# Kernel tuning notes

Measured on AMD Instinct MI355X. Metric: run time of the kernel, lower is better.

## Reference

```python
import jax, jax.numpy as jnp
import numpy as np

EPS = 1e-4
TAU = 0.1
GAMMA = 64.0
RADIUS = 1.0
N_HEADS = 4
N_SPLIT = 4


def _l2norm(x, axis=-1):
    return x / jnp.maximum(jnp.linalg.norm(x, axis=axis, keepdims=True), 1e-12)


def _pd2(a, b):
    # pairwise squared distances: (B,N,M)
    return (jnp.sum(a * a, -1)[:, :, None] + jnp.sum(b * b, -1)[:, None, :]
            - 2.0 * jnp.einsum('bnd,bmd->bnm', a, b))


def _sim_matrix(xyz, nf, radius, gamma):
    # radius-masked Gaussian feature affinity, zero diagonal
    N = xyz.shape[1]
    d2x = _pd2(xyz, xyz)
    d2f = _pd2(nf, nf)
    A = jnp.exp(-gamma * d2f / nf.shape[-1]) * (d2x < radius * radius).astype(nf.dtype)
    return A * (1.0 - jnp.eye(N, dtype=A.dtype))


def _norm_lap(A, eps):
    deg = A.sum(-1)
    dinv = jax.lax.rsqrt(deg + eps)
    na = A * dinv[:, :, None] * dinv[:, None, :]
    lap = jnp.eye(A.shape[1], dtype=A.dtype) - na
    return lap, na


def _mincut(X, na, W1, b1, W2, b2, tau):
    # one GCN layer + temperature softmax soft assignment; pooled = weighted mean
    h = jax.nn.relu(jnp.einsum('bnm,bmc->bnc', na, X) @ W1 + b1)
    s = jax.nn.softmax((h @ W2 + b2) / tau, axis=-1)  # (B,N,K)
    denom = s.sum(1)[:, :, None] + EPS                # (B,K,1)
    c_fea = jnp.einsum('bnk,bnc->bkc', s, X) / denom
    return c_fea, s


def _centers(xyz, s):
    denom = s.sum(1)[:, :, None] + EPS
    return jnp.einsum('bnk,bnd->bkd', s, xyz) / denom


def _assignment_loss(p_xyz, c_xyz, s):
    d2 = _pd2(p_xyz, c_xyz)
    return jnp.mean(jnp.sum(s * d2, -1))


def _welsch(p_xyz, c_xyz, sigma):
    d2min = jnp.min(_pd2(p_xyz, c_xyz), -1)
    return jnp.mean(1.0 - jnp.exp(-d2min / (2.0 * sigma * sigma)))


def _knn_affinity(xyz, k):
    N = xyz.shape[1]
    d2 = _pd2(xyz, xyz)
    eye = jnp.eye(N, dtype=d2.dtype)
    neg = -(d2 + 1e6 * eye)
    thresh = jax.lax.top_k(neg, k)[0][..., -1:]
    mask = (neg >= thresh).astype(d2.dtype)
    A = jnp.exp(-d2) * mask * (1.0 - eye)
    return jnp.maximum(A, jnp.swapaxes(A, 1, 2))


def _cut_loss(na, xyz, alpha):
    N = xyz.shape[1]
    lap = jnp.eye(N, dtype=na.dtype) - na
    quad = jnp.einsum('bnd,bnm,bmd->b', xyz, lap, xyz)
    return alpha * jnp.mean(quad / N)


def _cross_attn(gf, cf, Wq, Wk, Wv, Wo, n_heads):
    B, N, C = gf.shape
    M = cf.shape[1]
    dh = C // n_heads
    q = (gf @ Wq).reshape(B, N, n_heads, dh)
    k = (cf @ Wk).reshape(B, M, n_heads, dh)
    v = (cf @ Wv).reshape(B, M, n_heads, dh)
    scores = jnp.einsum('bnhd,bmhd->bhnm', q, k) / np.sqrt(dh).astype(np.float32)
    attn = jax.nn.softmax(scores, -1)
    out = jnp.einsum('bhnm,bmhd->bnhd', attn, v).reshape(B, N, C) @ Wo
    return out, attn.mean(1)


def setup_inputs() -> dict:
    key = jax.random.key(0)
    ks = jax.random.split(key, 20)
    B, N_sp, C, H, K = 2, 1024, 256, 128, 64
    Kg = K // N_SPLIT
    sc = 1.0 / np.sqrt(C)
    sh = 1.0 / np.sqrt(H)
    return {
        'g_fea': jax.random.normal(ks[0], (B, N_sp, C), jnp.float32),
        'g_xyz': jax.random.uniform(ks[1], (B, N_sp, 3), jnp.float32),
        'p_fea_0': jax.random.normal(ks[2], (B, 4096, C), jnp.float32),
        'p_xyz_0': jax.random.uniform(ks[3], (B, 4096, 3), jnp.float32),
        'p_fea_1': jax.random.normal(ks[4], (B, 2048, C), jnp.float32),
        'p_xyz_1': jax.random.uniform(ks[5], (B, 2048, 3), jnp.float32),
        'lW1': jax.random.normal(ks[6], (C, H), jnp.float32) * sc,
        'lb1': jnp.zeros((H,), jnp.float32),
        'lW2': jax.random.normal(ks[7], (H, K), jnp.float32) * sh,
        'lb2': jnp.zeros((K,), jnp.float32),
        'gW1': jax.random.normal(ks[8], (C, H), jnp.float32) * sc,
        'gb1': jnp.zeros((H,), jnp.float32),
        'gW2': jax.random.normal(ks[9], (H, Kg), jnp.float32) * sh,
        'gb2': jnp.zeros((Kg,), jnp.float32),
        'Wq': jax.random.normal(ks[10], (C, C), jnp.float32) * sc,
        'Wk': jax.random.normal(ks[11], (C, C), jnp.float32) * sc,
        'Wv': jax.random.normal(ks[12], (C, C), jnp.float32) * sc,
        'Wo': jax.random.normal(ks[13], (C, C), jnp.float32) * sc,
    }


def reference(g_fea, g_xyz, p_fea_0, p_xyz_0, p_fea_1, p_xyz_1,
              lW1, lb1, lW2, lb2, gW1, gb1, gW2, gb2, Wq, Wk, Wv, Wo):
    l_loss = jnp.zeros((), jnp.float32)
    cx_list, cf_list = [], []
    for p_xyz_i, p_fea_i in ((p_xyz_0, p_fea_0), (p_xyz_1, p_fea_1)):
        nf = _l2norm(p_fea_i)
        A = _sim_matrix(p_xyz_i, nf, RADIUS, GAMMA)
        na = _norm_lap(A, EPS)[1]
        c_fea_i, s_i = _mincut(p_fea_i, na, lW1, lb1, lW2, lb2, TAU)
        c_xyz_i = _centers(p_xyz_i, s_i)
        c2p = jnp.einsum('bnk,bkc->bnc', s_i, jax.lax.stop_gradient(c_fea_i))
        l_loss = l_loss + _assignment_loss(p_xyz_i, c_xyz_i, s_i)
        l_loss = l_loss + jnp.linalg.norm(_l2norm(c2p) - nf) + _welsch(p_xyz_i, c_xyz_i, 1.0)
        cx_list.append(c_xyz_i)
        cf_list.append(c_fea_i)
    c_xyz = jnp.concatenate(cx_list, 1)
    c_fea = jnp.concatenate(cf_list, 1)
    A_c = _knn_affinity(c_xyz, 2 * N_SPLIT)
    na_c = _norm_lap(A_c, EPS)[1]
    c_fea_g, gs = _mincut(c_fea, na_c, gW1, gb1, gW2, gb2, TAU)
    c_xyz_g = _centers(c_xyz, gs)
    cut_loss_c = _assignment_loss(c_xyz, c_xyz_g, gs)
    agg, G_t = _cross_attn(g_fea, c_fea_g, Wq, Wk, Wv, Wo, N_HEADS)
    A_g = _sim_matrix(g_xyz, _l2norm(g_fea), 4.0 * RADIUS, GAMMA)
    ass_loss = _cut_loss(_norm_lap(A_g, EPS)[1], g_xyz, 1e-4)
    g_loss = jnp.mean(jnp.sum(jnp.linalg.norm(_l2norm(agg) - _l2norm(g_fea), axis=-1), 1)) + ass_loss
    return agg, l_loss + cut_loss_c, g_loss
```

## Files before the change

### kernel.cpp

```cpp
#include <hip/hip_runtime.h>

#define EPSF 1e-4f

typedef __attribute__((ext_vector_type(8))) short bf16x8;
typedef __attribute__((ext_vector_type(4))) float f32x4;

__device__ __forceinline__ unsigned short f2bf(float f){
    unsigned int u = __float_as_uint(f);
    return (unsigned short)((u + 0x7FFF + ((u >> 16) & 1)) >> 16);
}
__device__ __forceinline__ float bf2f(unsigned short u){
    return __uint_as_float(((unsigned int)u) << 16);
}
__device__ __forceinline__ float waveSum(float v){
    #pragma unroll
    for (int o = 32; o; o >>= 1) v += __shfl_xor(v, o, 64);
    return v;
}
__device__ __forceinline__ float waveMin(float v){
    #pragma unroll
    for (int o = 32; o; o >>= 1) v = fminf(v, __shfl_xor(v, o, 64));
    return v;
}
__device__ __forceinline__ float waveMax(float v){
    #pragma unroll
    for (int o = 32; o; o >>= 1) v = fmaxf(v, __shfl_xor(v, o, 64));
    return v;
}
__device__ __forceinline__ float blockReduceSum(float v, float* red, int nthr){
    int t = threadIdx.x;
    red[t] = v; __syncthreads();
    for (int s = nthr >> 1; s > 0; s >>= 1){
        if (t < s) red[t] += red[t + s];
        __syncthreads();
    }
    float r = red[0]; __syncthreads();
    return r;
}

__global__ void l2norm_kernel(const float* __restrict__ x, unsigned short* __restrict__ outb, int rows){
    __shared__ float red[256];
    int row = blockIdx.x, t = threadIdx.x;
    float v = x[(long)row*256 + t];
    float s = blockReduceSum(v*v, red, 256);
    float nrm = fmaxf(sqrtf(s), 1e-12f);
    outb[(long)row*256 + t] = f2bf(v / nrm);
}

__global__ void cvt_bf16_kernel(const float* __restrict__ in, unsigned short* __restrict__ out, long n4){
    long i = (long)blockIdx.x*256 + threadIdx.x;
    if (i < n4){
        float4 v = ((const float4*)in)[i];
        unsigned int lo = f2bf(v.x) | ((unsigned int)f2bf(v.y) << 16);
        unsigned int hi = f2bf(v.z) | ((unsigned int)f2bf(v.w) << 16);
        uint2 u; u.x = lo; u.y = hi;
        ((uint2*)out)[i] = u;
    }
}

__global__ void tcvt_kernel(const float* __restrict__ W, unsigned short* __restrict__ WT,
                            int Rw, int Cw){
    __shared__ float tile[64][65];
    int r0 = blockIdx.x*64, c0 = blockIdx.y*64;
    int t = threadIdx.x;
    for (int idx = t; idx < 4096; idx += 256){
        int rr = idx >> 6, cc = idx & 63;
        tile[rr][cc] = (r0+rr < Rw && c0+cc < Cw) ? W[(long)(r0+rr)*Cw + c0+cc] : 0.f;
    }
    __syncthreads();
    for (int idx = t; idx < 4096; idx += 256){
        int cc = idx >> 6, rr = idx & 63;
        if (r0+rr < Rw && c0+cc < Cw)
            WT[(long)(c0+cc)*Rw + r0+rr] = f2bf(tile[rr][cc]);
    }
}

__global__ __launch_bounds__(256) void gram_mfma_kernel(const unsigned short* __restrict__ nf,
                                                        const float* __restrict__ xyz,
                                                        unsigned short* __restrict__ A,
                                                        float* __restrict__ deg,
                                                        int N, float r2, float scale){
    __shared__ short tA[128*40], tB[128*40];
    __shared__ float xa[384], xb[384];
    int tid = threadIdx.x;
    int n0 = blockIdx.y*128, m0 = blockIdx.x*128;
    for (int i = tid; i < 384; i += 256){ xa[i] = xyz[n0*3 + i]; xb[i] = xyz[m0*3 + i]; }
    int w = tid >> 6, l = tid & 63;
    int wy = w >> 1, wx = w & 1;
    int lg = l >> 4, lr = l & 15;
    int srow = tid >> 2, sc = tid & 3;
    f32x4 zero = {0.f, 0.f, 0.f, 0.f};
    f32x4 acc[4][4];
    #pragma unroll
    for (int i = 0; i < 4; ++i)
        #pragma unroll
        for (int j = 0; j < 4; ++j) acc[i][j] = zero;
    for (int kt = 0; kt < 256; kt += 32){
        __syncthreads();
        #pragma unroll
        for (int p = 0; p < 2; ++p){
            int row = srow + p*64;
            uint4 va = *(const uint4*)(nf + (long)(n0+row)*256 + kt + sc*8);
            uint4 vb = *(const uint4*)(nf + (long)(m0+row)*256 + kt + sc*8);
            *(uint4*)(tA + row*40 + sc*8) = va;
            *(uint4*)(tB + row*40 + sc*8) = vb;
        }
        __syncthreads();
        bf16x8 af[4], bfr[4];
        #pragma unroll
        for (int f = 0; f < 4; ++f){
            af[f]  = *(const bf16x8*)(tA + (wy*64 + f*16 + lr)*40 + lg*8);
            bfr[f] = *(const bf16x8*)(tB + (wx*64 + f*16 + lr)*40 + lg*8);
        }
        #pragma unroll
        for (int i = 0; i < 4; ++i)
            #pragma unroll
            for (int j = 0; j < 4; ++j)
                acc[i][j] = __builtin_amdgcn_mfma_f32_16x16x32_bf16(af[i], bfr[j], acc[i][j], 0, 0, 0);
    }
    #pragma unroll
    for (int fi = 0; fi < 4; ++fi){
        #pragma unroll
        for (int r = 0; r < 4; ++r){
            int n_ = wy*64 + fi*16 + lg*4 + r;
            int gn = n0 + n_;
            float rowacc = 0.f;
            #pragma unroll
            for (int fj = 0; fj < 4; ++fj){
                int m_ = wx*64 + fj*16 + lr;
                float dx = xa[n_*3+0]-xb[m_*3+0];
                float dy = xa[n_*3+1]-xb[m_*3+1];
                float dz = xa[n_*3+2]-xb[m_*3+2];
                float d2x = dx*dx + dy*dy + dz*dz;
                int gm = m0 + m_;
                float dot = acc[fi][fj][r];
                float val = (d2x < r2 && gn != gm) ? expf(scale*(2.f*dot - 2.f)) : 0.f;
                A[(long)gn*N + gm] = f2bf(val);
                rowacc += val;
            }
            rowacc += __shfl_xor(rowacc, 1, 64);
            rowacc += __shfl_xor(rowacc, 2, 64);
            rowacc += __shfl_xor(rowacc, 4, 64);
            rowacc += __shfl_xor(rowacc, 8, 64);
            if (lr == 0) atomicAdd(&deg[gn], rowacc);
        }
    }
}

__global__ __launch_bounds__(256) void transpose_scale_kernel(const float* __restrict__ fea,
                                                              const float* __restrict__ deg,
                                                              unsigned short* __restrict__ feaT,
                                                              unsigned short* __restrict__ xsT, int N){
    __shared__ float tile[64][65];
    __shared__ float dl[64];
    int m0 = blockIdx.x*64, c0 = blockIdx.y*64;
    int t = threadIdx.x;
    int lr = t >> 2, lc = (t & 3)*16;
    #pragma unroll
    for (int j = 0; j < 4; ++j){
        float4 v = *(const float4*)(fea + (long)(m0+lr)*256 + c0 + lc + j*4);
        tile[lr][lc+j*4+0] = v.x; tile[lr][lc+j*4+1] = v.y;
        tile[lr][lc+j*4+2] = v.z; tile[lr][lc+j*4+3] = v.w;
    }
    if (t < 64) dl[t] = rsqrtf(deg[m0+t] + EPSF);
    __syncthreads();
    unsigned short vr[16] __attribute__((aligned(16)));
    unsigned short vs[16] __attribute__((aligned(16)));
    #pragma unroll
    for (int j = 0; j < 16; ++j){
        float raw = tile[lc+j][lr];
        vr[j] = f2bf(raw);
        vs[j] = f2bf(raw * dl[lc+j]);
    }
    long off = (long)(c0+lr)*N + m0 + lc;
    *(uint4*)(feaT + off)     = *(uint4*)&vr[0];
    *(uint4*)(feaT + off + 8) = *(uint4*)&vr[8];
    *(uint4*)(xsT + off)      = *(uint4*)&vs[0];
    *(uint4*)(xsT + off + 8)  = *(uint4*)&vs[8];
}

__global__ __launch_bounds__(256) void ax_mfma_kernel(const unsigned short* __restrict__ A,
                                                      const unsigned short* __restrict__ xsT,
                                                      float* __restrict__ PY, int N, int split){
    __shared__ short tA[128*40], tB[64*40];
    int tid = threadIdx.x;
    int c0 = blockIdx.x*64, n0 = blockIdx.y*128;
    int chunk = blockIdx.z;
    int L = N/split, kbase = chunk*L, kend = kbase + L;
    int w = tid >> 6, l = tid & 63;
    int wy = w >> 1, wx = w & 1;
    int lg = l >> 4, lr = l & 15;
    int srow = tid >> 2, sc = tid & 3;
    f32x4 zero = {0.f, 0.f, 0.f, 0.f};
    f32x4 acc[4][2];
    #pragma unroll
    for (int i = 0; i < 4; ++i)
        #pragma unroll
        for (int j = 0; j < 2; ++j) acc[i][j] = zero;
    uint4 pva[2], pvb;
    #pragma unroll
    for (int p = 0; p < 2; ++p)
        pva[p] = *(const uint4*)(A + (long)(n0+srow+p*64)*N + kbase + sc*8);
    pvb = *(const uint4*)(xsT + (long)(c0+srow)*N + kbase + sc*8);
    for (int kt = kbase; kt < kend; kt += 32){
        __syncthreads();
        #pragma unroll
        for (int p = 0; p < 2; ++p)
            *(uint4*)(tA + (srow+p*64)*40 + sc*8) = pva[p];
        *(uint4*)(tB + srow*40 + sc*8) = pvb;
        __syncthreads();
        if (kt + 32 < kend){
            #pragma unroll
            for (int p = 0; p < 2; ++p)
                pva[p] = *(const uint4*)(A + (long)(n0+srow+p*64)*N + kt + 32 + sc*8);
            pvb = *(const uint4*)(xsT + (long)(c0+srow)*N + kt + 32 + sc*8);
        }
        bf16x8 af[4], bfr[2];
        #pragma unroll
        for (int f = 0; f < 4; ++f)
            af[f] = *(const bf16x8*)(tA + (wy*64 + f*16 + lr)*40 + lg*8);
        #pragma unroll
        for (int f = 0; f < 2; ++f)
            bfr[f] = *(const bf16x8*)(tB + (wx*32 + f*16 + lr)*40 + lg*8);
        #pragma unroll
        for (int i = 0; i < 4; ++i)
            #pragma unroll
            for (int j = 0; j < 2; ++j)
                acc[i][j] = __builtin_amdgcn_mfma_f32_16x16x32_bf16(af[i], bfr[j], acc[i][j], 0, 0, 0);
    }
    float* out = PY + (long)chunk*N*256;
    #pragma unroll
    for (int fi = 0; fi < 4; ++fi){
        #pragma unroll
        for (int fj = 0; fj < 2; ++fj){
            #pragma unroll
            for (int r = 0; r < 4; ++r){
                int n_ = n0 + wy*64 + fi*16 + lg*4 + r;
                int c_ = c0 + wx*32 + fj*16 + lr;
                out[(long)n_*256 + c_] = acc[fi][fj][r];
            }
        }
    }
}

__global__ void combine_kernel(const float* __restrict__ PY, const float* __restrict__ deg,
                               unsigned short* __restrict__ Yb, int N, int split){
    long i = (long)blockIdx.x*256 + threadIdx.x;
    long e = i*8;
    float4 s0 = {0,0,0,0}, s1 = {0,0,0,0};
    for (int q = 0; q < split; ++q){
        const float4* p = (const float4*)(PY + (long)q*N*256 + e);
        float4 a = p[0], b = p[1];
        s0.x += a.x; s0.y += a.y; s0.z += a.z; s0.w += a.w;
        s1.x += b.x; s1.y += b.y; s1.z += b.z; s1.w += b.w;
    }
    float d = rsqrtf(deg[e >> 8] + EPSF);
    unsigned short vb[8] __attribute__((aligned(16)));
    vb[0] = f2bf(s0.x*d); vb[1] = f2bf(s0.y*d);
    vb[2] = f2bf(s0.z*d); vb[3] = f2bf(s0.w*d);
    vb[4] = f2bf(s1.x*d); vb[5] = f2bf(s1.y*d);
    vb[6] = f2bf(s1.z*d); vb[7] = f2bf(s1.w*d);
    *(uint4*)(Yb + e) = *(uint4*)vb;
}

__global__ __launch_bounds__(256) void gemm_XW_mfma_kernel(const unsigned short* __restrict__ X,
                                                           const unsigned short* __restrict__ WT,
                                                           const float* __restrict__ bias,
                                                           float* __restrict__ outF,
                                                           unsigned short* __restrict__ outB,
                                                           int R, int Ci, int Co, int relu){
    __shared__ short tA[128*40], tB[128*40];
    int tid = threadIdx.x;
    int c0 = blockIdx.x*128, r0 = blockIdx.y*128;
    int w = tid >> 6, l = tid & 63;
    int wy = w >> 1, wx = w & 1;
    int lg = l >> 4, lr = l & 15;
    int srow = tid >> 2, sc = tid & 3;
    f32x4 zero = {0.f, 0.f, 0.f, 0.f};
    f32x4 acc[4][4];
    #pragma unroll
    for (int i = 0; i < 4; ++i)
        #pragma unroll
        for (int j = 0; j < 4; ++j) acc[i][j] = zero;
    uint4 pva[2], pvb[2];
    #pragma unroll
    for (int p = 0; p < 2; ++p){
        int row = srow + p*64;
        int ar = r0 + row, br = c0 + row;
        pva[p] = (ar < R)  ? *(const uint4*)(X  + (long)ar*Ci + sc*8) : (uint4){0,0,0,0};
        pvb[p] = (br < Co) ? *(const uint4*)(WT + (long)br*Ci + sc*8) : (uint4){0,0,0,0};
    }
    for (int kt = 0; kt < Ci; kt += 32){
        __syncthreads();
        #pragma unroll
        for (int p = 0; p < 2; ++p){
            int row = srow + p*64;
            *(uint4*)(tA + row*40 + sc*8) = pva[p];
            *(uint4*)(tB + row*40 + sc*8) = pvb[p];
        }
        __syncthreads();
        if (kt + 32 < Ci){
            #pragma unroll
            for (int p = 0; p < 2; ++p){
                int row = srow + p*64;
                int ar = r0 + row, br = c0 + row;
                pva[p] = (ar < R)  ? *(const uint4*)(X  + (long)ar*Ci + kt + 32 + sc*8) : (uint4){0,0,0,0};
                pvb[p] = (br < Co) ? *(const uint4*)(WT + (long)br*Ci + kt + 32 + sc*8) : (uint4){0,0,0,0};
            }
        }
        bf16x8 af[4], bfr[4];
        #pragma unroll
        for (int f = 0; f < 4; ++f){
            af[f]  = *(const bf16x8*)(tA + (wy*64 + f*16 + lr)*40 + lg*8);
            bfr[f] = *(const bf16x8*)(tB + (wx*64 + f*16 + lr)*40 + lg*8);
        }
        #pragma unroll
        for (int i = 0; i < 4; ++i)
            #pragma unroll
            for (int j = 0; j < 4; ++j)
                acc[i][j] = __builtin_amdgcn_mfma_f32_16x16x32_bf16(af[i], bfr[j], acc[i][j], 0, 0, 0);
    }
    #pragma unroll
    for (int fi = 0; fi < 4; ++fi){
        #pragma unroll
        for (int fj = 0; fj < 4; ++fj){
            #pragma unroll
            for (int r = 0; r < 4; ++r){
                int rr = r0 + wy*64 + fi*16 + lg*4 + r;
                int cc = c0 + wx*64 + fj*16 + lr;
                if (rr < R && cc < Co){
                    float v = acc[fi][fj][r] + (bias ? bias[cc] : 0.f);
                    if (relu) v = fmaxf(v, 0.f);
                    if (outF) outF[(long)rr*Co + cc] = v;
                    if (outB) outB[(long)rr*Co + cc] = f2bf(v);
                }
            }
        }
    }
}

__global__ __launch_bounds__(256) void gemm_splitk_kernel(const float* __restrict__ X,
                                                          const float* __restrict__ W0,
                                                          const float* __restrict__ W1,
                                                          float* __restrict__ part,
                                                          int R, int Ci, int Co, int Ks){
    __shared__ float sa[32][65], sb[32][65];
    int tid = threadIdx.x, tx = tid & 15, ty = tid >> 4;
    int c0 = blockIdx.x * 64, r0 = blockIdx.y * 64;
    int z = blockIdx.z;
    const float* W = (z / Ks) ? W1 : W0;
    int kchunk = Ci / Ks, kst = (z % Ks) * kchunk;
    float acc[4][4] = {};
    for (int kt = kst; kt < kst + kchunk; kt += 32){
        #pragma unroll
        for (int p = 0; p < 8; ++p){
            int idx = p*256 + tid;
            int k = idx & 31, i = idx >> 5;
            int rr = r0 + i;
            sa[k][i] = (rr < R) ? X[(long)rr*Ci + kt + k] : 0.f;
            int j = idx & 63, kk = idx >> 6;
            int cc = c0 + j;
            sb[kk][j] = (cc < Co) ? W[(long)(kt+kk)*Co + cc] : 0.f;
        }
        __syncthreads();
        #pragma unroll
        for (int k = 0; k < 32; ++k){
            float a0=sa[k][ty*4+0],a1=sa[k][ty*4+1],a2=sa[k][ty*4+2],a3=sa[k][ty*4+3];
            float b0=sb[k][tx*4+0],b1=sb[k][tx*4+1],b2=sb[k][tx*4+2],b3=sb[k][tx*4+3];
            acc[0][0]+=a0*b0; acc[0][1]+=a0*b1; acc[0][2]+=a0*b2; acc[0][3]+=a0*b3;
            acc[1][0]+=a1*b0; acc[1][1]+=a1*b1; acc[1][2]+=a1*b2; acc[1][3]+=a1*b3;
            acc[2][0]+=a2*b0; acc[2][1]+=a2*b1; acc[2][2]+=a2*b2; acc[2][3]+=a2*b3;
            acc[3][0]+=a3*b0; acc[3][1]+=a3*b1; acc[3][2]+=a3*b2; acc[3][3]+=a3*b3;
        }
        __syncthreads();
    }
    float* outp = part + (long)z*R*Co;
    #pragma unroll
    for (int r = 0; r < 4; ++r){
        #pragma unroll
        for (int c = 0; c < 4; ++c){
            int rr = r0 + ty*4 + r, cc = c0 + tx*4 + c;
            if (rr < R && cc < Co) outp[(long)rr*Co + cc] = acc[r][c];
        }
    }
}

__global__ void combine_bias_kernel(const float* __restrict__ part, const float* __restrict__ bias,
                                    float* __restrict__ out, int R, int Co, int Ks, int relu){
    long i = (long)blockIdx.x*256 + threadIdx.x;
    if (i < (long)R*Co){
        long zs = (long)R*Co;
        float s = 0.f;
        for (int q = 0; q < Ks; ++q) s += part[q*zs + i];
        float v = s + (bias ? bias[i % Co] : 0.f);
        if (relu) v = fmaxf(v, 0.f);
        out[i] = v;
    }
}

__global__ __launch_bounds__(256) void softmaxT_kernel(float* __restrict__ s,
                                                       unsigned short* __restrict__ sT,
                                                       int sStride, float invtau){
    __shared__ unsigned short st[64][65];
    int blk = blockIdx.x, t = threadIdx.x, w = t >> 6, l = t & 63;
    #pragma unroll
    for (int i = 0; i < 16; ++i){
        int rloc = w + 4*i;
        long row = (long)blk*64 + rloc;
        float v = s[row*64 + l] * invtau;
        float mx = waveMax(v);
        float e = expf(v - mx);
        float sum = waveSum(e);
        float p = e / sum;
        s[row*64 + l] = p;
        st[l][rloc] = f2bf(p);
    }
    __syncthreads();
    int k = t >> 2, j = (t & 3)*16;
    unsigned short vbuf[16] __attribute__((aligned(16)));
    #pragma unroll
    for (int q = 0; q < 16; ++q) vbuf[q] = st[k][j+q];
    long off = (long)k*sStride + (long)blk*64 + j;
    *(uint4*)(sT + off)     = *(uint4*)&vbuf[0];
    *(uint4*)(sT + off + 8) = *(uint4*)&vbuf[8];
}

__global__ __launch_bounds__(256) void stx_mfma_kernel(const unsigned short* __restrict__ sT,
                                                       const unsigned short* __restrict__ feaT,
                                                       float* __restrict__ part,
                                                       int N, int split, int sStride){
    __shared__ short tA[64*40], tB[256*40];
    int tid = threadIdx.x;
    int z = blockIdx.x, b = z / split, chunk = z % split;
    int L = N / split, kst = chunk * L;
    const unsigned short* sTb = sT + (long)b*N;
    const unsigned short* fT  = feaT + (long)b*256*N;
    int w = tid >> 6, l = tid & 63;
    int lg = l >> 4, lr = l & 15;
    f32x4 zero = {0.f, 0.f, 0.f, 0.f};
    f32x4 acc[4][4];
    #pragma unroll
    for (int i = 0; i < 4; ++i)
        #pragma unroll
        for (int j = 0; j < 4; ++j) acc[i][j] = zero;
    int srow = tid >> 2, koff = (tid & 3)*8;
    for (int kt = kst; kt < kst + L; kt += 32){
        __syncthreads();
        *(uint4*)(tA + srow*40 + koff) = *(const uint4*)(sTb + (long)srow*sStride + kt + koff);
        #pragma unroll
        for (int p = 0; p < 4; ++p){
            int row = srow + p*64;
            *(uint4*)(tB + row*40 + koff) = *(const uint4*)(fT + (long)row*N + kt + koff);
        }
        __syncthreads();
        bf16x8 af[4], bfr[4];
        #pragma unroll
        for (int f = 0; f < 4; ++f){
            af[f]  = *(const bf16x8*)(tA + (f*16 + lr)*40 + lg*8);
            bfr[f] = *(const bf16x8*)(tB + (w*64 + f*16 + lr)*40 + lg*8);
        }
        #pragma unroll
        for (int i = 0; i < 4; ++i)
            #pragma unroll
            for (int j = 0; j < 4; ++j)
                acc[i][j] = __builtin_amdgcn_mfma_f32_16x16x32_bf16(af[i], bfr[j], acc[i][j], 0, 0, 0);
    }
    float* outp = part + (long)z*64*256;
    #pragma unroll
    for (int fi = 0; fi < 4; ++fi){
        #pragma unroll
        for (int fj = 0; fj < 4; ++fj){
            #pragma unroll
            for (int r = 0; r < 4; ++r){
                int kc = fi*16 + lg*4 + r;
                int cc = w*64 + fj*16 + lr;
                outp[(long)kc*256 + cc] = acc[fi][fj][r];
            }
        }
    }
}

__global__ void softmax_kernel(float* __restrict__ x, int Kc, float tau){
    int row = blockIdx.x, lane = threadIdx.x;
    bool act = lane < Kc;
    float v = act ? x[(long)row*Kc + lane] / tau : -1e30f;
    float mx = v;
    #pragma unroll
    for (int o = 32; o; o >>= 1) mx = fmaxf(mx, __shfl_xor(mx, o, 64));
    float e = act ? expf(v - mx) : 0.f;
    float s = e;
    #pragma unroll
    for (int o = 32; o; o >>= 1) s += __shfl_xor(s, o, 64);
    if (act) x[(long)row*Kc + lane] = e / s;
}

__global__ void cluster_xyz_kernel(const float* __restrict__ s, const float* __restrict__ xyz,
                                   float* __restrict__ outx, float* __restrict__ outd,
                                   int N, int Kc, int xBS, int dBS){
    __shared__ float red[256];
    int b = blockIdx.y, k = blockIdx.x, t = threadIdx.x;
    s   += (long)b*N*Kc;
    xyz += (long)b*N*3;
    float a0=0,a1=0,a2=0,ad=0;
    for (int n = t; n < N; n += 256){
        float sv = s[(long)n*Kc + k];
        ad += sv;
        a0 += sv*xyz[n*3+0]; a1 += sv*xyz[n*3+1]; a2 += sv*xyz[n*3+2];
    }
    a0 = blockReduceSum(a0, red, 256);
    a1 = blockReduceSum(a1, red, 256);
    a2 = blockReduceSum(a2, red, 256);
    ad = blockReduceSum(ad, red, 256);
    if (t == 0){
        outx[b*xBS + k*3+0] = a0;
        outx[b*xBS + k*3+1] = a1;
        outx[b*xBS + k*3+2] = a2;
        outd[b*dBS + k] = ad;
    }
}

__global__ __launch_bounds__(256) void gemm_sTX_kernel(const float* __restrict__ s,
                                                       const float* __restrict__ X,
                                                       float* __restrict__ part,
                                                       int N, int Kc, int split,
                                                       long sBS, long xBS){
    __shared__ float sa[32][65], sb[32][65];
    int tid = threadIdx.x, tx = tid & 15, ty = tid >> 4;
    int c0 = blockIdx.x * 64;
    int b = blockIdx.z / split, chunk = blockIdx.z % split;
    int L = N / split, nst = chunk * L;
    s += b*sBS; X += b*xBS;
    float* out = part + (long)blockIdx.z * Kc * 256;
    float acc[4][4] = {};
    for (int nt = nst; nt < nst + L; nt += 32){
        #pragma unroll
        for (int p = 0; p < 8; ++p){
            int idx = p*256 + tid;
            int i = idx & 63, k = idx >> 6;
            sa[k][i] = (i < Kc) ? s[(long)(nt+k)*Kc + i] : 0.f;
            int j = idx & 63, kk = idx >> 6;
            sb[kk][j] = X[(long)(nt+kk)*256 + c0 + j];
        }
        __syncthreads();
        #pragma unroll
        for (int k = 0; k < 32; ++k){
            float a0=sa[k][ty*4+0],a1=sa[k][ty*4+1],a2=sa[k][ty*4+2],a3=sa[k][ty*4+3];
            float b0=sb[k][tx*4+0],b1=sb[k][tx*4+1],b2=sb[k][tx*4+2],b3=sb[k][tx*4+3];
            acc[0][0]+=a0*b0; acc[0][1]+=a0*b1; acc[0][2]+=a0*b2; acc[0][3]+=a0*b3;
            acc[1][0]+=a1*b0; acc[1][1]+=a1*b1; acc[1][2]+=a1*b2; acc[1][3]+=a1*b3;
            acc[2][0]+=a2*b0; acc[2][1]+=a2*b1; acc[2][2]+=a2*b2; acc[2][3]+=a2*b3;
            acc[3][0]+=a3*b0; acc[3][1]+=a3*b1; acc[3][2]+=a3*b2; acc[3][3]+=a3*b3;
        }
        __syncthreads();
    }
    #pragma unroll
    for (int r = 0; r < 4; ++r){
        int kc = ty*4 + r;
        if (kc < Kc){
            #pragma unroll
            for (int c = 0; c < 4; ++c)
                out[(long)kc*256 + c0 + tx*4 + c] = acc[r][c];
        }
    }
}

__global__ void divide_sum_kernel(const float* __restrict__ part, const float* __restrict__ den,
                                  float* __restrict__ cfea, float* __restrict__ cxyz,
                                  int Kc, int split, int fBS, int xBS, int dBS){
    int b = blockIdx.y, k = blockIdx.x, t = threadIdx.x;
    float d = den[b*dBS + k] + EPSF;
    float s = 0.f;
    for (int q = 0; q < split; ++q)
        s += part[((long)(b*split+q)*Kc + k)*256 + t];
    cfea[(long)b*fBS + k*256 + t] = s / d;
    if (t < 3) cxyz[b*xBS + k*3 + t] /= d;
}

__global__ __launch_bounds__(256) void level_loss_kernel(const float* __restrict__ s,
                                                         const float* __restrict__ pxyz,
                                                         const float* __restrict__ cxyz,
                                                         const float* __restrict__ cfea,
                                                         const unsigned short* __restrict__ nfb,
                                                         float* __restrict__ scal,
                                                         int N, float inv, int ndsSlot){
    __shared__ float cf[64*256];
    __shared__ float cx[192];
    __shared__ float partA[4], partN[4];
    int b = blockIdx.y, t = threadIdx.x, w = t >> 6, l = t & 63;
    s    += (long)b*N*64;
    pxyz += (long)b*N*3;
    nfb  += (long)b*N*256;
    cxyz += (long)b*384;
    cfea += (long)b*32768;
    for (int i = t; i < 4096; i += 256)
        ((float4*)cf)[i] = ((const float4*)cfea)[i];
    if (t < 192) cx[t] = cxyz[t];
    __syncthreads();
    int n = blockIdx.x*4 + w;
    float sl = s[(long)n*64 + l];
    float px = pxyz[n*3+0], py = pxyz[n*3+1], pz = pxyz[n*3+2];
    float dx = px - cx[l*3+0], dy = py - cx[l*3+1], dz = pz - cx[l*3+2];
    float d2 = dx*dx + dy*dy + dz*dz;
    float assSum = waveSum(sl*d2);
    float dmin = waveMin(d2);
    float c0=0,c1=0,c2=0,c3=0;
    #pragma unroll 8
    for (int k = 0; k < 64; ++k){
        float sk = __shfl(sl, k, 64);
        const float* row = cf + k*256;
        c0 += sk*row[l]; c1 += sk*row[l+64]; c2 += sk*row[l+128]; c3 += sk*row[l+192];
    }
    float nrm2 = waveSum(c0*c0 + c1*c1 + c2*c2 + c3*c3);
    float inrm = 1.f / fmaxf(sqrtf(nrm2), 1e-12f);
    const unsigned short* nfr = nfb + (long)n*256;
    float e0 = c0*inrm - bf2f(nfr[l]);
    float e1 = c1*inrm - bf2f(nfr[l+64]);
    float e2 = c2*inrm - bf2f(nfr[l+128]);
    float e3 = c3*inrm - bf2f(nfr[l+192]);
    float nds = waveSum(e0*e0 + e1*e1 + e2*e2 + e3*e3);
    if (l == 0){
        partA[w] = inv*(assSum + 1.f - expf(-0.5f*dmin));
        partN[w] = nds;
    }
    __syncthreads();
    if (t == 0){
        int slot = blockIdx.x & 63;
        atomicAdd(&scal[slot], partA[0]+partA[1]+partA[2]+partA[3]);
        atomicAdd(&scal[ndsSlot*64 + slot], partN[0]+partN[1]+partN[2]+partN[3]);
    }
}

__global__ __launch_bounds__(128) void knn_nac_kernel(const float* __restrict__ cxyz,
                                                      float* __restrict__ nac){
    __shared__ float d2s[128][129];
    __shared__ float x[128][3];
    __shared__ float di[128];
    int b = blockIdx.x, n = threadIdx.x;
    x[n][0] = cxyz[b*384 + n*3+0];
    x[n][1] = cxyz[b*384 + n*3+1];
    x[n][2] = cxyz[b*384 + n*3+2];
    __syncthreads();
    float xn0 = x[n][0], xn1 = x[n][1], xn2 = x[n][2];
    for (int m = 0; m < 128; ++m){
        float dx = xn0-x[m][0], dy = xn1-x[m][1], dz = xn2-x[m][2];
        d2s[n][m] = dx*dx+dy*dy+dz*dz + (m==n ? 1e6f : 0.f);
    }
    float last = -1.f;
    for (int p = 0; p < 8; ++p){
        float cur = 1e30f;
        for (int m = 0; m < 128; ++m){
            float v = d2s[n][m];
            if (v > last && v < cur) cur = v;
        }
        last = cur;
    }
    for (int m = 0; m < 128; ++m){
        float d2 = d2s[n][m];
        d2s[n][m] = (m != n && d2 <= last) ? expf(-d2) : 0.f;
    }
    __syncthreads();
    for (int m = 0; m < 128; ++m){
        float v = fmaxf(d2s[n][m], d2s[m][n]);
        d2s[n][m] = v;
    }
    __syncthreads();
    float deg = 0.f;
    for (int m = 0; m < 128; ++m) deg += d2s[n][m];
    di[n] = rsqrtf(deg + EPSF);
    __syncthreads();
    float* Ab = nac + (long)b*16384;
    for (int c = 0; c < 128; ++c)
        Ab[c*128 + n] = d2s[c][n] * di[c] * di[n];
}

__global__ void bmm_small_kernel(const float* __restrict__ nac, const float* __restrict__ cfea,
                                 float* __restrict__ Y2){
    __shared__ float row[128];
    int b = blockIdx.y, n = blockIdx.x, t = threadIdx.x;
    if (t < 128) row[t] = nac[(long)b*16384 + n*128 + t];
    __syncthreads();
    float acc = 0.f;
    #pragma unroll 4
    for (int k = 0; k < 128; ++k) acc += row[k]*cfea[(long)b*32768 + k*256 + t];
    Y2[(long)b*32768 + n*256 + t] = acc;
}

__global__ void cutc_kernel(const float* __restrict__ gs, const float* __restrict__ cxyz,
                            const float* __restrict__ cxyzg, float* __restrict__ scal, float inv){
    __shared__ float cg[48];
    __shared__ float red[128];
    int b = blockIdx.x, t = threadIdx.x;
    if (t < 48) cg[t] = cxyzg[b*48 + t];
    __syncthreads();
    float x0 = cxyz[b*384 + t*3+0], x1 = cxyz[b*384 + t*3+1], x2 = cxyz[b*384 + t*3+2];
    float acc = 0.f;
    #pragma unroll
    for (int k = 0; k < 16; ++k){
        float dx = x0-cg[k*3+0], dy = x1-cg[k*3+1], dz = x2-cg[k*3+2];
        acc += gs[b*2048 + t*16 + k]*(dx*dx+dy*dy+dz*dz);
    }
    acc = blockReduceSum(acc, red, 128);
    if (t == 0) atomicAdd(&scal[b], acc*inv);
}

__global__ __launch_bounds__(256) void attn_kernel(const float* __restrict__ q,
                                                   const float* __restrict__ kk,
                                                   const float* __restrict__ vv,
                                                   unsigned short* __restrict__ aob){
    __shared__ float Ks[16][256], Vs[16][256];
    int b = blockIdx.y, n = blockIdx.x, t = threadIdx.x;
    #pragma unroll
    for (int p = 0; p < 16; ++p){
        int j = p*256 + t;
        Ks[j>>8][j&255] = kk[b*4096 + j];
        Vs[j>>8][j&255] = vv[b*4096 + j];
    }
    __syncthreads();
    float qv = q[((long)b*1024 + n)*256 + t];
    float sc[16];
    #pragma unroll
    for (int m = 0; m < 16; ++m){
        float v = qv * Ks[m][t];
        #pragma unroll
        for (int o = 32; o; o >>= 1) v += __shfl_xor(v, o, 64);
        sc[m] = v * 0.125f;
    }
    float mx = -1e30f;
    #pragma unroll
    for (int m = 0; m < 16; ++m) mx = fmaxf(mx, sc[m]);
    float sum = 0.f;
    #pragma unroll
    for (int m = 0; m < 16; ++m){ sc[m] = expf(sc[m]-mx); sum += sc[m]; }
    float o = 0.f;
    #pragma unroll
    for (int m = 0; m < 16; ++m) o += sc[m]*Vs[m][t];
    aob[((long)b*1024 + n)*256 + t] = f2bf(o / sum);
}

__global__ void quad_kernel(const unsigned short* __restrict__ A, const float* __restrict__ deg,
                            const float* __restrict__ xyz, float* __restrict__ scal){
    __shared__ float part[4];
    int t = threadIdx.x, w = t >> 6, l = t & 63;
    int n = blockIdx.x*4 + w;
    float a0=0,a1=0,a2=0;
    #pragma unroll 4
    for (int i = 0; i < 16; ++i){
        int m = l + i*64;
        float wv = bf2f(A[(long)n*1024 + m])*rsqrtf(deg[m] + EPSF);
        a0 += wv*xyz[m*3+0]; a1 += wv*xyz[m*3+1]; a2 += wv*xyz[m*3+2];
    }
    a0 = waveSum(a0); a1 = waveSum(a1); a2 = waveSum(a2);
    if (l == 0){
        float x0 = xyz[n*3+0], x1 = xyz[n*3+1], x2 = xyz[n*3+2];
        float dn = rsqrtf(deg[n] + EPSF);
        part[w] = (x0*x0+x1*x1+x2*x2) - dn*(x0*a0+x1*a1+x2*a2);
    }
    __syncthreads();
    if (t == 0) atomicAdd(&scal[4*64 + (blockIdx.x & 63)], part[0]+part[1]+part[2]+part[3]);
}

__global__ void gloss_kernel(const float* __restrict__ agg, const float* __restrict__ gfea,
                             float* __restrict__ scal){
    __shared__ float part[4];
    int t = threadIdx.x, w = t >> 6, l = t & 63;
    long r = (long)blockIdx.x*4 + w;
    const float* a = agg + r*256;
    const float* g = gfea + r*256;
    float a0=a[l],a1=a[l+64],a2=a[l+128],a3=a[l+192];
    float g0=g[l],g1=g[l+64],g2=g[l+128],g3=g[l+192];
    float na2 = waveSum(a0*a0+a1*a1+a2*a2+a3*a3);
    float ng2 = waveSum(g0*g0+g1*g1+g2*g2+g3*g3);
    float ia = 1.f/fmaxf(sqrtf(na2), 1e-12f), ig = 1.f/fmaxf(sqrtf(ng2), 1e-12f);
    float e0=a0*ia-g0*ig, e1=a1*ia-g1*ig, e2=a2*ia-g2*ig, e3=a3*ia-g3*ig;
    float d2 = waveSum(e0*e0+e1*e1+e2*e2+e3*e3);
    if (l == 0) part[w] = sqrtf(d2);
    __syncthreads();
    if (t == 0) atomicAdd(&scal[3*64 + (blockIdx.x & 63)], part[0]+part[1]+part[2]+part[3]);
}

__global__ void finalize_kernel(const float* __restrict__ scal, float* __restrict__ out){
    int t = threadIdx.x;
    float s[5];
    #pragma unroll
    for (int q = 0; q < 5; ++q){
        float v = scal[q*64 + t];
        #pragma unroll
        for (int o = 32; o; o >>= 1) v += __shfl_xor(v, o, 64);
        s[q] = v;
    }
    if (t == 0){
        out[524288] = s[0] + sqrtf(s[1]) + sqrtf(s[2]);
        out[524289] = s[3]*0.5f + 1e-4f*s[4]/2048.0f;
    }
}

extern "C" void kernel_launch(void* const* d_in, const int* in_sizes, int n_in,
                              void* d_out, int out_size, void* d_ws, size_t ws_size,
                              hipStream_t stream){
    const float* g_fea   = (const float*)d_in[0];
    const float* g_xyz   = (const float*)d_in[1];
    const float* p_fea_0 = (const float*)d_in[2];
    const float* p_xyz_0 = (const float*)d_in[3];
    const float* p_fea_1 = (const float*)d_in[4];
    const float* p_xyz_1 = (const float*)d_in[5];
    const float* lW1 = (const float*)d_in[6];
    const float* lb1 = (const float*)d_in[7];
    const float* lW2 = (const float*)d_in[8];
    const float* lb2 = (const float*)d_in[9];
    const float* gW1 = (const float*)d_in[10];
    const float* gb1 = (const float*)d_in[11];
    const float* gW2 = (const float*)d_in[12];
    const float* gb2 = (const float*)d_in[13];
    const float* Wq = (const float*)d_in[14];
    const float* Wk = (const float*)d_in[15];
    const float* Wv = (const float*)d_in[16];
    const float* Wo = (const float*)d_in[17];
    float* out = (float*)d_out;
    float* ws_f = (float*)d_ws;

    constexpr long O_SCALS = 0;
    constexpr long O_DEG   = 512;
    constexpr long O_CFEA  = 16384;
    constexpr long O_CXYZ  = 81920;
    constexpr long O_DEN   = 82688;
    constexpr long O_CFG   = 82944;
    constexpr long O_CXG   = 91136;
    constexpr long O_DENG  = 91232;
    constexpr long O_NFB   = 91296;
    constexpr long O_XST   = O_NFB  + 1572864;
    constexpr long O_FEAT  = O_XST  + 1048576;
    constexpr long O_YB    = O_FEAT + 1572864;
    constexpr long O_HB    = O_YB   + 1572864;
    constexpr long O_S     = O_HB   + 786432;
    constexpr long O_ST    = O_S    + 786432;
    constexpr long O_PY    = O_ST   + 393216;
    constexpr long O_A     = O_PY   + 8388608;
    constexpr long O_Q     = O_A    + 8388608;
    constexpr long O_GFB   = O_Q    + 524288;
    constexpr long O_AOB   = O_GFB  + 262144;
    constexpr long O_KK    = O_AOB  + 262144;
    constexpr long O_VV    = O_KK   + 8192;
    constexpr long O_NAC   = O_VV   + 8192;
    constexpr long O_Y2    = O_NAC  + 32768;
    constexpr long O_H2    = O_Y2   + 65536;
    constexpr long O_LG2   = O_H2   + 32768;
    constexpr long O_W1T   = O_LG2  + 4096;
    constexpr long O_W2T   = O_W1T  + 16384;
    constexpr long O_WQT   = O_W2T  + 4096;
    constexpr long O_WOT   = O_WQT  + 32768;

    hipMemsetAsync(ws_f + O_SCALS, 0, (512 + 14336)*sizeof(float), stream);

    unsigned short* nfb  = (unsigned short*)(ws_f + O_NFB);
    unsigned short* xsT  = (unsigned short*)(ws_f + O_XST);
    unsigned short* feaT = (unsigned short*)(ws_f + O_FEAT);
    unsigned short* Ybb  = (unsigned short*)(ws_f + O_YB);
    unsigned short* Hb   = (unsigned short*)(ws_f + O_HB);
    unsigned short* sTb  = (unsigned short*)(ws_f + O_ST);
    unsigned short* A    = (unsigned short*)(ws_f + O_A);
    unsigned short* gfb  = (unsigned short*)(ws_f + O_GFB);
    unsigned short* aob  = (unsigned short*)(ws_f + O_AOB);
    unsigned short* lW1T = (unsigned short*)(ws_f + O_W1T);
    unsigned short* lW2T = (unsigned short*)(ws_f + O_W2T);
    unsigned short* WqT  = (unsigned short*)(ws_f + O_WQT);
    unsigned short* WoT  = (unsigned short*)(ws_f + O_WOT);
    float* sb   = ws_f + O_S;
    float* degA = ws_f + O_DEG;
    float* PY   = ws_f + O_PY;
    float* Qf   = ws_f + O_Q;

    tcvt_kernel<<<dim3(4, 2), 256, 0, stream>>>(lW1, lW1T, 256, 128);
    tcvt_kernel<<<dim3(2, 1), 256, 0, stream>>>(lW2, lW2T, 128, 64);
    tcvt_kernel<<<dim3(4, 4), 256, 0, stream>>>(Wq, WqT, 256, 256);
    tcvt_kernel<<<dim3(4, 4), 256, 0, stream>>>(Wo, WoT, 256, 256);
    cvt_bf16_kernel<<<512, 256, 0, stream>>>(g_fea, gfb, 131072);

    struct Lvl { const float* fea; const float* xyz; int N; int k0; int ndsSlot; long degBase;
                 long rowOff; long featOff; };
    Lvl lv[2] = {{p_fea_0, p_xyz_0, 4096, 0, 1, 0, 0, 0},
                 {p_fea_1, p_xyz_1, 2048, 64, 2, 8192, 8192, 2097152}};

    for (int L = 0; L < 2; ++L){
        int N = lv[L].N;
        const float* fea = lv[L].fea;
        const float* xyz = lv[L].xyz;
        unsigned short* nfbL  = nfb + lv[L].rowOff*256;
        unsigned short* feaTL = feaT + lv[L].featOff;
        l2norm_kernel<<<2*N, 256, 0, stream>>>(fea, nfbL, 2*N);
        for (int b = 0; b < 2; ++b){
            float* degb = degA + lv[L].degBase + (long)b*N;
            gram_mfma_kernel<<<dim3(N/128, N/128), 256, 0, stream>>>(nfbL + (long)b*N*256,
                                                                     xyz + (long)b*N*3, A, degb,
                                                                     N, 1.0f, 0.25f);
            transpose_scale_kernel<<<dim3(N/64, 4), 256, 0, stream>>>(fea + (long)b*N*256, degb,
                                                                      feaTL + (long)b*256*N,
                                                                      xsT + (long)b*256*N, N);
            ax_mfma_kernel<<<dim3(4, N/128, 8), 256, 0, stream>>>(A, xsT + (long)b*256*N, PY, N, 8);
            combine_kernel<<<N/8, 256, 0, stream>>>(PY, degb,
                                                    Ybb + (lv[L].rowOff + (long)b*N)*256, N, 8);
        }
    }

    gemm_XW_mfma_kernel<<<dim3(1, 96), 256, 0, stream>>>(Ybb, lW1T, lb1, nullptr, Hb,
                                                         12288, 256, 128, 1);
    gemm_XW_mfma_kernel<<<dim3(1, 96), 256, 0, stream>>>(Hb, lW2T, lb2, sb, nullptr,
                                                         12288, 128, 64, 0);
    softmaxT_kernel<<<192, 256, 0, stream>>>(sb, sTb, 12288, 10.0f);

    for (int L = 0; L < 2; ++L){
        int N = lv[L].N;
        const float* xyz = lv[L].xyz;
        float* sL = sb + lv[L].rowOff*64;
        cluster_xyz_kernel<<<dim3(64, 2), 256, 0, stream>>>(sL, xyz, ws_f + O_CXYZ + lv[L].k0*3,
                                                            ws_f + O_DEN + lv[L].k0, N, 64, 384, 128);
        stx_mfma_kernel<<<32, 256, 0, stream>>>(sTb + lv[L].rowOff, feaT + lv[L].featOff,
                                                PY, N, 16, 12288);
        divide_sum_kernel<<<dim3(64, 2), 256, 0, stream>>>(PY, ws_f + O_DEN + lv[L].k0,
                                                           ws_f + O_CFEA + lv[L].k0*256,
                                                           ws_f + O_CXYZ + lv[L].k0*3,
                                                           64, 16, 128*256, 384, 128);
        level_loss_kernel<<<dim3(N/4, 2), 256, 0, stream>>>(sL, xyz, ws_f + O_CXYZ + lv[L].k0*3,
                                                            ws_f + O_CFEA + lv[L].k0*256,
                                                            nfb + lv[L].rowOff*256,
                                                            ws_f + O_SCALS, N, 1.0f/(2.0f*N), lv[L].ndsSlot);
    }

    knn_nac_kernel<<<2, 128, 0, stream>>>(ws_f + O_CXYZ, ws_f + O_NAC);
    bmm_small_kernel<<<dim3(128, 2), 256, 0, stream>>>(ws_f + O_NAC, ws_f + O_CFEA, ws_f + O_Y2);
    gemm_splitk_kernel<<<dim3(2, 4, 4), 256, 0, stream>>>(ws_f + O_Y2, gW1, nullptr, PY,
                                                          256, 256, 128, 4);
    combine_bias_kernel<<<128, 256, 0, stream>>>(PY, gb1, ws_f + O_H2, 256, 128, 4, 1);
    gemm_splitk_kernel<<<dim3(1, 4, 4), 256, 0, stream>>>(ws_f + O_H2, gW2, nullptr, PY,
                                                          256, 128, 16, 4);
    combine_bias_kernel<<<16, 256, 0, stream>>>(PY, gb2, ws_f + O_LG2, 256, 16, 4, 0);
    softmax_kernel<<<256, 64, 0, stream>>>(ws_f + O_LG2, 16, 0.1f);
    cluster_xyz_kernel<<<dim3(16, 2), 256, 0, stream>>>(ws_f + O_LG2, ws_f + O_CXYZ,
                                                        ws_f + O_CXG, ws_f + O_DENG, 128, 16, 48, 16);
    gemm_sTX_kernel<<<dim3(4, 1, 8), 256, 0, stream>>>(ws_f + O_LG2, ws_f + O_CFEA, PY,
                                                       128, 16, 4, 128L*16, 128L*256);
    divide_sum_kernel<<<dim3(16, 2), 256, 0, stream>>>(PY, ws_f + O_DENG, ws_f + O_CFG,
                                                       ws_f + O_CXG, 16, 4, 16*256, 48, 16);
    cutc_kernel<<<2, 128, 0, stream>>>(ws_f + O_LG2, ws_f + O_CXYZ, ws_f + O_CXG,
                                       ws_f + O_SCALS, 1.0f/256.0f);

    gemm_XW_mfma_kernel<<<dim3(2, 16), 256, 0, stream>>>(gfb, WqT, nullptr, Qf, nullptr,
                                                         2048, 256, 256, 0);
    gemm_splitk_kernel<<<dim3(4, 1, 16), 256, 0, stream>>>(ws_f + O_CFG, Wk, Wv, PY,
                                                           32, 256, 256, 8);
    combine_bias_kernel<<<32, 256, 0, stream>>>(PY, nullptr, ws_f + O_KK, 32, 256, 8, 0);
    combine_bias_kernel<<<32, 256, 0, stream>>>(PY + 8L*32*256, nullptr, ws_f + O_VV, 32, 256, 8, 0);
    attn_kernel<<<dim3(1024, 2), 256, 0, stream>>>(Qf, ws_f + O_KK, ws_f + O_VV, aob);
    gemm_XW_mfma_kernel<<<dim3(2, 16), 256, 0, stream>>>(aob, WoT, nullptr, out, nullptr,
                                                         2048, 256, 256, 0);

    l2norm_kernel<<<2048, 256, 0, stream>>>(g_fea, nfb, 2048);
    for (int b = 0; b < 2; ++b){
        float* degb = degA + 12288 + (long)b*1024;
        gram_mfma_kernel<<<dim3(8, 8), 256, 0, stream>>>(nfb + (long)b*1024*256, g_xyz + (long)b*1024*3,
                                                         A, degb, 1024, 16.0f, 0.25f);
        quad_kernel<<<256, 256, 0, stream>>>(A, degb, g_xyz + (long)b*1024*3, ws_f + O_SCALS);
    }

    gloss_kernel<<<512, 256, 0, stream>>>(out, g_fea, ws_f + O_SCALS);
    finalize_kernel<<<1, 64, 0, stream>>>(ws_f + O_SCALS, out);
}
```

Measured before the change: 756.8 us.

## Widen A·X tile to 128 columns and store split-K partials as bf16

The A·X MFMA kernel now computes a 128x128 output tile per block instead of 128x64. That halves how often the large affinity matrix A is read across column blocks and doubles the MFMA work per LDS fill. Split-K partial sums are staged through shared memory and written as bf16 with coalesced 16-byte stores, and combine_kernel reads them as bf16, which halves partial-sum traffic. The cost is more accumulator registers, which may lower occupancy, and some precision lost by rounding each partial to bf16 before the sum.

Result: faster. 739.1 us (-2.3%).

```diff
diff --git a/kernel.cpp b/kernel.cpp
--- a/kernel.cpp
+++ b/kernel.cpp
@@ -181,10 +181,12 @@
 
 __global__ __launch_bounds__(256) void ax_mfma_kernel(const unsigned short* __restrict__ A,
                                                       const unsigned short* __restrict__ xsT,
-                                                      float* __restrict__ PY, int N, int split){
-    __shared__ short tA[128*40], tB[64*40];
+                                                      unsigned short* __restrict__ PYb, int N, int split){
+    __shared__ short smem[16384];
+    short* tA = smem;
+    short* tB = smem + 5120;
     int tid = threadIdx.x;
-    int c0 = blockIdx.x*64, n0 = blockIdx.y*128;
+    int c0 = blockIdx.x*128, n0 = blockIdx.y*128;
     int chunk = blockIdx.z;
     int L = N/split, kbase = chunk*L, kend = kbase + L;
     int w = tid >> 6, l = tid & 63;
@@ -192,74 +194,89 @@
     int lg = l >> 4, lr = l & 15;
     int srow = tid >> 2, sc = tid & 3;
     f32x4 zero = {0.f, 0.f, 0.f, 0.f};
-    f32x4 acc[4][2];
+    f32x4 acc[4][4];
     #pragma unroll
     for (int i = 0; i < 4; ++i)
         #pragma unroll
-        for (int j = 0; j < 2; ++j) acc[i][j] = zero;
-    uint4 pva[2], pvb;
-    #pragma unroll
-    for (int p = 0; p < 2; ++p)
-        pva[p] = *(const uint4*)(A + (long)(n0+srow+p*64)*N + kbase + sc*8);
-    pvb = *(const uint4*)(xsT + (long)(c0+srow)*N + kbase + sc*8);
+        for (int j = 0; j < 4; ++j) acc[i][j] = zero;
+    uint4 pva[2], pvb[2];
+    #pragma unroll
+    for (int p = 0; p < 2; ++p){
+        int row = srow + p*64;
+        pva[p] = *(const uint4*)(A   + (long)(n0+row)*N + kbase + sc*8);
+        pvb[p] = *(const uint4*)(xsT + (long)(c0+row)*N + kbase + sc*8);
+    }
     for (int kt = kbase; kt < kend; kt += 32){
         __syncthreads();
         #pragma unroll
-        for (int p = 0; p < 2; ++p)
-            *(uint4*)(tA + (srow+p*64)*40 + sc*8) = pva[p];
-        *(uint4*)(tB + srow*40 + sc*8) = pvb;
+        for (int p = 0; p < 2; ++p){
+            int row = srow + p*64;
+            *(uint4*)(tA + row*40 + sc*8) = pva[p];
+            *(uint4*)(tB + row*40 + sc*8) = pvb[p];
+        }
         __syncthreads();
         if (kt + 32 < kend){
             #pragma unroll
-            for (int p = 0; p < 2; ++p)
-                pva[p] = *(const uint4*)(A + (long)(n0+srow+p*64)*N + kt + 32 + sc*8);
-            pvb = *(const uint4*)(xsT + (long)(c0+srow)*N + kt + 32 + sc*8);
-        }
-        bf16x8 af[4], bfr[2];
-        #pragma unroll
-        for (int f = 0; f < 4; ++f)
-            af[f] = *(const bf16x8*)(tA + (wy*64 + f*16 + lr)*40 + lg*8);
-        #pragma unroll
-        for (int f = 0; f < 2; ++f)
-            bfr[f] = *(const bf16x8*)(tB + (wx*32 + f*16 + lr)*40 + lg*8);
+            for (int p = 0; p < 2; ++p){
+                int row = srow + p*64;
+                pva[p] = *(const uint4*)(A   + (long)(n0+row)*N + kt + 32 + sc*8);
+                pvb[p] = *(const uint4*)(xsT + (long)(c0+row)*N + kt + 32 + sc*8);
+            }
+        }
+        bf16x8 af[4], bfr[4];
+        #pragma unroll
+        for (int f = 0; f < 4; ++f){
+            af[f]  = *(const bf16x8*)(tA + (wy*64 + f*16 + lr)*40 + lg*8);
+            bfr[f] = *(const bf16x8*)(tB + (wx*64 + f*16 + lr)*40 + lg*8);
+        }
         #pragma unroll
         for (int i = 0; i < 4; ++i)
             #pragma unroll
-            for (int j = 0; j < 2; ++j)
+            for (int j = 0; j < 4; ++j)
                 acc[i][j] = __builtin_amdgcn_mfma_f32_16x16x32_bf16(af[i], bfr[j], acc[i][j], 0, 0, 0);
     }
-    float* out = PY + (long)chunk*N*256;
+    __syncthreads();
+    unsigned short* ot = (unsigned short*)smem;
     #pragma unroll
     for (int fi = 0; fi < 4; ++fi){
         #pragma unroll
-        for (int fj = 0; fj < 2; ++fj){
+        for (int fj = 0; fj < 4; ++fj){
             #pragma unroll
             for (int r = 0; r < 4; ++r){
-                int n_ = n0 + wy*64 + fi*16 + lg*4 + r;
-                int c_ = c0 + wx*32 + fj*16 + lr;
-                out[(long)n_*256 + c_] = acc[fi][fj][r];
+                int n_ = wy*64 + fi*16 + lg*4 + r;
+                int c_ = wx*64 + fj*16 + lr;
+                ot[n_*128 + c_] = f2bf(acc[fi][fj][r]);
             }
         }
     }
-}
-
-__global__ void combine_kernel(const float* __restrict__ PY, const float* __restrict__ deg,
+    __syncthreads();
+    unsigned short* outp = PYb + (long)chunk*N*256;
+    #pragma unroll
+    for (int q = 0; q < 8; ++q){
+        int idx = q*256 + tid;
+        int row = idx >> 4, coff = (idx & 15)*8;
+        *(uint4*)(outp + (long)(n0+row)*256 + c0 + coff) = *(const uint4*)(ot + row*128 + coff);
+    }
+}
+
+__global__ void combine_kernel(const unsigned short* __restrict__ PYb, const float* __restrict__ deg,
                                unsigned short* __restrict__ Yb, int N, int split){
     long i = (long)blockIdx.x*256 + threadIdx.x;
     long e = i*8;
-    float4 s0 = {0,0,0,0}, s1 = {0,0,0,0};
+    float s[8] = {0,0,0,0,0,0,0,0};
     for (int q = 0; q < split; ++q){
-        const float4* p = (const float4*)(PY + (long)q*N*256 + e);
-        float4 a = p[0], b = p[1];
-        s0.x += a.x; s0.y += a.y; s0.z += a.z; s0.w += a.w;
-        s1.x += b.x; s1.y += b.y; s1.z += b.z; s1.w += b.w;
+        uint4 u = *(const uint4*)(PYb + (long)q*N*256 + e);
+        unsigned int ww[4] = {u.x, u.y, u.z, u.w};
+        #pragma unroll
+        for (int j = 0; j < 4; ++j){
+            s[2*j]   += __uint_as_float(ww[j] << 16);
+            s[2*j+1] += __uint_as_float(ww[j] & 0xFFFF0000u);
+        }
     }
     float d = rsqrtf(deg[e >> 8] + EPSF);
     unsigned short vb[8] __attribute__((aligned(16)));
-    vb[0] = f2bf(s0.x*d); vb[1] = f2bf(s0.y*d);
-    vb[2] = f2bf(s0.z*d); vb[3] = f2bf(s0.w*d);
-    vb[4] = f2bf(s1.x*d); vb[5] = f2bf(s1.y*d);
-    vb[6] = f2bf(s1.z*d); vb[7] = f2bf(s1.w*d);
+    #pragma unroll
+    for (int j = 0; j < 8; ++j) vb[j] = f2bf(s[j]*d);
     *(uint4*)(Yb + e) = *(uint4*)vb;
 }
 
@@ -867,6 +884,7 @@
     float* sb   = ws_f + O_S;
     float* degA = ws_f + O_DEG;
     float* PY   = ws_f + O_PY;
+    unsigned short* PYb = (unsigned short*)(ws_f + O_PY);
     float* Qf   = ws_f + O_Q;
 
     tcvt_kernel<<<dim3(4, 2), 256, 0, stream>>>(lW1, lW1T, 256, 128);
@@ -895,8 +913,8 @@
             transpose_scale_kernel<<<dim3(N/64, 4), 256, 0, stream>>>(fea + (long)b*N*256, degb,
                                                                       feaTL + (long)b*256*N,
                                                                       xsT + (long)b*256*N, N);
-            ax_mfma_kernel<<<dim3(4, N/128, 8), 256, 0, stream>>>(A, xsT + (long)b*256*N, PY, N, 8);
-            combine_kernel<<<N/8, 256, 0, stream>>>(PY, degb,
+            ax_mfma_kernel<<<dim3(2, N/128, 8), 256, 0, stream>>>(A, xsT + (long)b*256*N, PYb, N, 8);
+            combine_kernel<<<N/8, 256, 0, stream>>>(PYb, degb,
                                                     Ybb + (lv[L].rowOff + (long)b*N)*256, N, 8);
         }
     }
```
